# Optimization experiments

Measured on AMD Instinct MI355X. Metric: run time of the kernel, lower is better.

## Reference

```python
import jax, jax.numpy as jnp
import numpy as np

TAU = 2.0
SUR_ALPHA = 4.0  # spikingjelly surrogate.Sigmoid default alpha
LN_EPS = 1e-5
SCALE = 0.125
NUM_HEADS = 16


@jax.custom_vjp
def _spike(u):
    return (u >= 0.0).astype(u.dtype)

def _spike_fwd(u):
    return _spike(u), u

def _spike_bwd(u, g):
    s = jax.nn.sigmoid(SUR_ALPHA * u)
    return (g * SUR_ALPHA * s * (1.0 - s),)

_spike.defvjp(_spike_fwd, _spike_bwd)


def lif(x, v_th=1.0):
    # Single-step LIF from fresh state v=0, v_reset=0:
    # v_post = v + (x - v)/tau = x/tau; spike = H(v_post - v_th)
    return _spike(x / TAU - v_th)


def ln(x, g, b):
    m = jnp.mean(x, axis=-1, keepdims=True)
    v = jnp.var(x, axis=-1, keepdims=True)
    return (x - m) * jax.lax.rsqrt(v + LN_EPS) * g + b


def setup_inputs() -> dict:
    key = jax.random.key(0)
    ks = jax.random.split(key, 8)
    B, L, D = 4, 1024, 1024
    HID = 4096
    s_d = 1.0 / np.sqrt(D)
    s_h = 1.0 / np.sqrt(HID)
    return {
        "x": jax.random.normal(ks[0], (B, L, D), jnp.float32),
        "q_w": jax.random.normal(ks[1], (D, D), jnp.float32) * s_d,
        "q_g": jnp.ones((D,), jnp.float32),
        "q_b": jnp.zeros((D,), jnp.float32),
        "k_w": jax.random.normal(ks[2], (D, D), jnp.float32) * s_d,
        "k_g": jnp.ones((D,), jnp.float32),
        "k_b": jnp.zeros((D,), jnp.float32),
        "v_w": jax.random.normal(ks[3], (D, D), jnp.float32) * s_d,
        "v_g": jnp.ones((D,), jnp.float32),
        "v_b": jnp.zeros((D,), jnp.float32),
        "proj_w": jax.random.normal(ks[4], (D, D), jnp.float32) * s_d,
        "proj_bias": jnp.zeros((D,), jnp.float32),
        "proj_g": jnp.ones((D,), jnp.float32),
        "proj_beta": jnp.zeros((D,), jnp.float32),
        "fc1_w": jax.random.normal(ks[5], (D, HID), jnp.float32) * s_d,
        "fc1_bias": jnp.zeros((HID,), jnp.float32),
        "fc1_g": jnp.ones((HID,), jnp.float32),
        "fc1_beta": jnp.zeros((HID,), jnp.float32),
        "fc2_w": jax.random.normal(ks[6], (HID, D), jnp.float32) * s_h,
        "fc2_bias": jnp.zeros((D,), jnp.float32),
        "fc2_g": jnp.ones((D,), jnp.float32),
        "fc2_beta": jnp.zeros((D,), jnp.float32),
    }


def reference(x, q_w, q_g, q_b, k_w, k_g, k_b, v_w, v_g, v_b,
              proj_w, proj_bias, proj_g, proj_beta,
              fc1_w, fc1_bias, fc1_g, fc1_beta,
              fc2_w, fc2_bias, fc2_g, fc2_beta):
    B, L, D = x.shape
    H = NUM_HEADS
    hd = D // H

    # --- SSA ---
    q = lif(ln(x @ q_w, q_g, q_b))  # (B,L,D), binary spikes
    k = lif(ln(x @ k_w, k_g, k_b))
    v = lif(ln(x @ v_w, v_g, v_b))
    q = q.reshape(B, L, H, hd).transpose(0, 2, 1, 3)  # (B,H,L,hd)
    k = k.reshape(B, L, H, hd).transpose(0, 2, 1, 3)
    v = v.reshape(B, L, H, hd).transpose(0, 2, 1, 3)

    attn = jnp.einsum('bhqd,bhkd->bhqk', q, k) * SCALE  # no softmax
    y = jnp.einsum('bhqk,bhkd->bhqd', attn, v)
    y = y.transpose(0, 2, 1, 3).reshape(B, L, D)
    y = lif(y, v_th=0.5)                    # attn_lif (v_threshold=0.5)
    y = lif(ln(y @ proj_w + proj_bias, proj_g, proj_beta))

    x = x + y  # residual 1

    # --- MLP ---
    m = lif(ln(x @ fc1_w + fc1_bias, fc1_g, fc1_beta))
    m = lif(ln(m @ fc2_w + fc2_bias, fc2_g, fc2_beta))

    return x + m  # residual 2
```

## Files before the change

### kernel.cpp

```cpp
#include <hip/hip_runtime.h>
#include <hip/hip_bf16.h>


#define NB 4
#define LL 1024
#define DIM 1024
#define NH 16
#define HDIM 64
#define HID 4096
#define NROWS (NB * LL)

typedef unsigned short u16;
typedef __attribute__((ext_vector_type(8))) short short8v;
typedef __attribute__((ext_vector_type(4))) float f32x4;

__device__ __forceinline__ u16 f2bf(float f) {
    unsigned u = __builtin_bit_cast(unsigned, f);
    return (u16)((u + 0x7fffu + ((u >> 16) & 1u)) >> 16);
}
__device__ __forceinline__ float bf2f(u16 h) {
    unsigned u = ((unsigned)h) << 16;
    return __builtin_bit_cast(float, u);
}
__device__ __forceinline__ void split3v(float v, u16& a, u16& b, u16& c) {
    a = f2bf(v);
    float r = v - bf2f(a);
    b = f2bf(r);
    float r2 = r - bf2f(b);
    c = f2bf(r2);
}

__global__ __launch_bounds__(256) void split3_rows(
    const float* __restrict__ X, u16* __restrict__ Xs, int K)
{
    const int row = blockIdx.y;
    const int c4 = (blockIdx.x * 256 + threadIdx.x) * 4;
    if (c4 >= K) return;
    float4 v = *(const float4*)(X + (size_t)row * K + c4);
    float vv[4] = {v.x, v.y, v.z, v.w};
    u16 h0[4], h1[4], h2[4];
#pragma unroll
    for (int j = 0; j < 4; ++j) split3v(vv[j], h0[j], h1[j], h2[j]);
    u16* base = Xs + (size_t)row * 3 * K + c4;
    *(uint2*)(base + 0 * K) = *(uint2*)h0;
    *(uint2*)(base + 1 * K) = *(uint2*)h1;
    *(uint2*)(base + 2 * K) = *(uint2*)h2;
}

__global__ __launch_bounds__(256) void split_wt(
    const float* __restrict__ W, u16* __restrict__ Wt, int K, int N, int ldwt)
{
    __shared__ float tile[64][65];
    const int k0 = blockIdx.y * 64, n0 = blockIdx.x * 64;
    const int t = threadIdx.x;
    const int rr = t >> 4;
    const int cc = (t & 15) * 4;
#pragma unroll
    for (int it = 0; it < 4; ++it) {
        const int k = rr + it * 16;
        float4 v = *(const float4*)(W + (size_t)(k0 + k) * N + n0 + cc);
        tile[cc + 0][k] = v.x; tile[cc + 1][k] = v.y;
        tile[cc + 2][k] = v.z; tile[cc + 3][k] = v.w;
    }
    __syncthreads();
    const int n = t >> 2, kc = (t & 3) * 16;
    u16 h0[16], h1[16], h2[16];
#pragma unroll
    for (int j = 0; j < 16; ++j)
        split3v(tile[n][kc + j], h0[j], h1[j], h2[j]);
    u16* base = Wt + (size_t)(n0 + n) * ldwt + k0 + kc;
    *(uint4*)(base + 0 * K)     = ((uint4*)h0)[0];
    *(uint4*)(base + 0 * K + 8) = ((uint4*)h0)[1];
    *(uint4*)(base + 1 * K)     = ((uint4*)h1)[0];
    *(uint4*)(base + 1 * K + 8) = ((uint4*)h1)[1];
    *(uint4*)(base + 2 * K)     = ((uint4*)h2)[0];
    *(uint4*)(base + 2 * K + 8) = ((uint4*)h2)[1];
}

#define AS1G const __attribute__((address_space(1))) void*
#define AS3L __attribute__((address_space(3))) void*

__global__ __launch_bounds__(512, 2) void gemm256(
    const u16* __restrict__ A, int lda,
    const u16* __restrict__ Bt, int ldb,
    unsigned apack, unsigned bpack, int nt,
    const float* __restrict__ bias,
    float* __restrict__ Out, int ldo)
{
    __shared__ u16 As2[2][16384];
    __shared__ u16 Bs2[2][16384];
    const int t = threadIdx.x;
    const int wid = t >> 6, lane = t & 63;
    const int wm = wid >> 2, wn = wid & 3;
    const int row0 = blockIdx.y * 256, col0 = blockIdx.x * 256;
    const int lrow = lane & 15, lk = lane >> 4;
    const int sr0 = t >> 3;
    const int scol = ((t & 7) ^ (sr0 & 7)) * 8;

    f32x4 acc[8][4];
#pragma unroll
    for (int i = 0; i < 8; ++i)
#pragma unroll
        for (int j = 0; j < 4; ++j) acc[i][j] = f32x4{0.f, 0.f, 0.f, 0.f};

#define STA(bs, Rb, c0)                                                        \
    __builtin_amdgcn_global_load_lds(                                          \
        (AS1G)(A + (size_t)(row0 + (Rb) + sr0) * lda + (c0) + scol),           \
        (AS3L)(&As2[bs][(Rb) * 64 + t * 8]), 16, 0, 0);
#define STB(bs, Rb, c0)                                                        \
    {                                                                          \
        const int _rho = (Rb) + sr0;                                           \
        const int _bc = ((_rho >> 5) & 3) * 64 + ((_rho >> 7) << 5) + (_rho & 31); \
        __builtin_amdgcn_global_load_lds(                                      \
            (AS1G)(Bt + (size_t)(col0 + _bc) * ldb + (c0) + scol),             \
            (AS3L)(&Bs2[bs][(Rb) * 64 + t * 8]), 16, 0, 0);                    \
    }
#define STPAIR0(bs, cA, cB) STA(bs, 0, cA)   STA(bs, 128, cA)
#define STPAIR1(bs, cA, cB) STB(bs, 0, cB)   STB(bs, 64, cB)
#define STPAIR2(bs, cA, cB) STA(bs, 64, cA)  STA(bs, 192, cA)
#define STPAIR3(bs, cA, cB) STB(bs, 128, cB) STB(bs, 192, cB)

#define VMW(n) asm volatile("s_waitcnt vmcnt(" #n ")" ::: "memory");
#define BAR  __builtin_amdgcn_s_barrier();
#define BARP                                                                   \
    __builtin_amdgcn_s_barrier();                                              \
    __builtin_amdgcn_sched_barrier(0);

#define PHASE(MQ, NQ, P, STAGES)                                               \
    {                                                                          \
        short8v af[4][2], bf[2][2];                                            \
        _Pragma("unroll")                                                      \
        for (int mf = 0; mf < 4; ++mf) {                                       \
            const int r = wm * 128 + (MQ) * 64 + mf * 16 + lrow;               \
            _Pragma("unroll")                                                  \
            for (int ks = 0; ks < 2; ++ks) {                                   \
                const int slot = (lk + ks * 4) ^ (r & 7);                      \
                af[mf][ks] = *(const short8v*)&As2[P][r * 64 + slot * 8];      \
            }                                                                  \
        }                                                                      \
        _Pragma("unroll")                                                      \
        for (int nf = 0; nf < 2; ++nf) {                                       \
            const int rho = (NQ) * 128 + (wn >> 1) * 64 + (wn & 1) * 32        \
                            + nf * 16 + lrow;                                  \
            _Pragma("unroll")                                                  \
            for (int ks = 0; ks < 2; ++ks) {                                   \
                const int slot = (lk + ks * 4) ^ (rho & 7);                    \
                bf[nf][ks] = *(const short8v*)&Bs2[P][rho * 64 + slot * 8];    \
            }                                                                  \
        }                                                                      \
        STAGES                                                                 \
        asm volatile("s_waitcnt lgkmcnt(0)" ::: "memory");                     \
        __builtin_amdgcn_sched_barrier(0);                                     \
        __builtin_amdgcn_s_setprio(1);                                         \
        _Pragma("unroll")                                                      \
        for (int mf = 0; mf < 4; ++mf)                                         \
            _Pragma("unroll")                                                  \
            for (int nf = 0; nf < 2; ++nf)                                     \
                _Pragma("unroll")                                              \
                for (int ks = 0; ks < 2; ++ks)                                 \
                    acc[(MQ) * 4 + mf][(NQ) * 2 + nf] =                        \
                        __builtin_amdgcn_mfma_f32_16x16x32_bf16(               \
                            af[mf][ks], bf[nf][ks],                            \
                            acc[(MQ) * 4 + mf][(NQ) * 2 + nf], 0, 0, 0);       \
        __builtin_amdgcn_s_setprio(0);                                         \
    }
#define NOSTAGE ((void)0);

    {
        const int cA = (apack & 15) * 1024;
        const int cB = (bpack & 15) * 1024;
        STPAIR0(0, cA, cB) STPAIR1(0, cA, cB)
        STPAIR2(0, cA, cB) STPAIR3(0, cA, cB)
    }

    for (int kt = 0; kt < nt - 1; ++kt) {
        const int p = kt & 1, np = p ^ 1;
        const int nkt = kt + 1;
        const int nns = nkt >> 4, nk0 = (nkt & 15) * 64;
        const int nA = (int)((apack >> (nns * 4)) & 15) * 1024 + nk0;
        const int nB = (int)((bpack >> (nns * 4)) & 15) * 1024 + nk0;
        VMW(4) BARP PHASE(0, 0, p, STPAIR0(np, nA, nB))
        VMW(4) BAR  PHASE(1, 0, p, STPAIR1(np, nA, nB))
        VMW(4) BAR  PHASE(1, 1, p, STPAIR2(np, nA, nB))
        BAR         PHASE(0, 1, p, STPAIR3(np, nA, nB))
    }
    {
        const int p = (nt - 1) & 1;
        VMW(4) BARP PHASE(0, 0, p, NOSTAGE)
        VMW(2) BAR  PHASE(1, 0, p, NOSTAGE)
        VMW(0) BAR  PHASE(1, 1, p, NOSTAGE)
        BAR         PHASE(0, 1, p, NOSTAGE)
    }
#undef STA
#undef STB
#undef STPAIR0
#undef STPAIR1
#undef STPAIR2
#undef STPAIR3
#undef VMW
#undef BAR
#undef BARP
#undef PHASE
#undef NOSTAGE

#pragma unroll
    for (int ni = 0; ni < 4; ++ni) {
        const int col = col0 + wn * 64 + ni * 16 + lrow;
        const float bv = bias ? bias[col] : 0.f;
#pragma unroll
        for (int mi = 0; mi < 8; ++mi) {
            const int rbase = row0 + wm * 128 + mi * 16 + lk * 4;
#pragma unroll
            for (int r = 0; r < 4; ++r)
                Out[(size_t)(rbase + r) * ldo + col] = acc[mi][ni][r] + bv;
        }
    }
}

struct SegList { int a[6]; int b[6]; int n; };

template <int BN_>
__global__ __launch_bounds__(256) void gemm_mfma(
    const u16* __restrict__ A, int lda,
    const u16* __restrict__ Bt, int ldb,
    SegList segs, int Kseg,
    const float* __restrict__ bias,
    float* __restrict__ Out, int ldo)
{
    constexpr int NF = BN_ / 32;
    __shared__ u16 As[128 * 64];
    __shared__ u16 Bs[BN_ * 64];
    const int t = threadIdx.x;
    const int wid = t >> 6, lane = t & 63;
    const int wr = wid >> 1, wc = wid & 1;
    const int row0 = blockIdx.y * 128, col0 = blockIdx.x * BN_;
    const int lrow = lane & 15;
    const int s_subrow = lane >> 3;
    const int s_slot   = (lane & 7) ^ (lane >> 3);
    const int s_coff   = s_slot * 8;

    f32x4 acc[4][NF];
#pragma unroll
    for (int i = 0; i < 4; ++i)
#pragma unroll
        for (int j = 0; j < NF; ++j) acc[i][j] = f32x4{0.f, 0.f, 0.f, 0.f};

    for (int s = 0; s < segs.n; ++s) {
        const u16* pa = A + segs.a[s];
        const u16* pb = Bt + segs.b[s];
        for (int k0 = 0; k0 < Kseg; k0 += 64) {
            asm volatile("s_waitcnt lgkmcnt(0)" ::: "memory");
            __syncthreads();
#pragma unroll
            for (int c = 0; c < 4; ++c) {
                const int chunk = wid * 4 + c;
                const int rg = row0 + chunk * 8 + s_subrow;
                __builtin_amdgcn_global_load_lds(
                    (AS1G)(pa + (size_t)rg * lda + k0 + s_coff),
                    (AS3L)(&As[chunk * 512 + lane * 8]), 16, 0, 0);
            }
#pragma unroll
            for (int c = 0; c < NF; ++c) {
                const int chunk = wid * NF + c;
                const int rg = col0 + chunk * 8 + s_subrow;
                __builtin_amdgcn_global_load_lds(
                    (AS1G)(pb + (size_t)rg * ldb + k0 + s_coff),
                    (AS3L)(&Bs[chunk * 512 + lane * 8]), 16, 0, 0);
            }
            asm volatile("s_waitcnt vmcnt(0)" ::: "memory");
            __syncthreads();
#pragma unroll
            for (int ksub = 0; ksub < 2; ++ksub) {
                short8v af[4], bfr[NF];
#pragma unroll
                for (int f = 0; f < 4; ++f) {
                    const int ra = wr * 64 + f * 16 + lrow;
                    const int slot = ((lane >> 4) + ksub * 4) ^ (lrow & 7);
                    af[f] = *(const short8v*)&As[ra * 64 + slot * 8];
                }
#pragma unroll
                for (int f = 0; f < NF; ++f) {
                    const int rb = wc * (BN_ / 2) + f * 16 + lrow;
                    const int slot = ((lane >> 4) + ksub * 4) ^ (lrow & 7);
                    bfr[f] = *(const short8v*)&Bs[rb * 64 + slot * 8];
                }
#pragma unroll
                for (int i = 0; i < 4; ++i)
#pragma unroll
                    for (int j = 0; j < NF; ++j)
                        acc[i][j] = __builtin_amdgcn_mfma_f32_16x16x32_bf16(
                            af[i], bfr[j], acc[i][j], 0, 0, 0);
            }
        }
    }
#pragma unroll
    for (int j = 0; j < NF; ++j) {
        const int col = col0 + wc * (BN_ / 2) + j * 16 + lrow;
        const float bv = bias ? bias[col] : 0.f;
#pragma unroll
        for (int i = 0; i < 4; ++i) {
            const int rbase = row0 + wr * 64 + i * 16 + (lane >> 4) * 4;
#pragma unroll
            for (int r = 0; r < 4; ++r)
                Out[(size_t)(rbase + r) * ldo + col] = acc[i][j][r] + bv;
        }
    }
}

template <int DN>
__global__ __launch_bounds__(256) void lnlif2(
    const float* __restrict__ U, int ld, int coloff,
    const float* __restrict__ g, const float* __restrict__ beta,
    const float* __restrict__ resid,
    u16* __restrict__ spike_bf16,
    float* __restrict__ out_f32,
    u16* __restrict__ split3_out)
{
    constexpr int PT = DN / 1024;
    const int r = blockIdx.x, t = threadIdx.x;
    const float4* u4 = (const float4*)(U + (size_t)r * ld + coloff);
    float4 vals[PT];
    float lsum = 0.f;
#pragma unroll
    for (int i = 0; i < PT; ++i) {
        vals[i] = u4[t + i * 256];
        lsum += (vals[i].x + vals[i].y) + (vals[i].z + vals[i].w);
    }
    __shared__ float red[4];
    __shared__ float bcast;
    for (int o = 32; o > 0; o >>= 1) lsum += __shfl_down(lsum, o);
    if ((t & 63) == 0) red[t >> 6] = lsum;
    __syncthreads();
    if (t == 0) bcast = (red[0] + red[1] + red[2] + red[3]) * (1.f / DN);
    __syncthreads();
    const float m = bcast;
    float lss = 0.f;
#pragma unroll
    for (int i = 0; i < PT; ++i) {
        float dx = vals[i].x - m, dy = vals[i].y - m;
        float dz = vals[i].z - m, dw = vals[i].w - m;
        lss += (dx * dx + dy * dy) + (dz * dz + dw * dw);
    }
    for (int o = 32; o > 0; o >>= 1) lss += __shfl_down(lss, o);
    if ((t & 63) == 0) red[t >> 6] = lss;
    __syncthreads();
    if (t == 0) bcast = (red[0] + red[1] + red[2] + red[3]) * (1.f / DN);
    __syncthreads();
    const float rs = 1.f / sqrtf(bcast + 1e-5f);
#pragma unroll
    for (int i = 0; i < PT; ++i) {
        const int c = (t + i * 256) * 4;
        const size_t idx = (size_t)r * DN + c;
        const float4 gg = *(const float4*)(g + c);
        const float4 bb = *(const float4*)(beta + c);
        float sv[4];
        sv[0] = ((vals[i].x - m) * rs * gg.x + bb.x >= 2.0f) ? 1.f : 0.f;
        sv[1] = ((vals[i].y - m) * rs * gg.y + bb.y >= 2.0f) ? 1.f : 0.f;
        sv[2] = ((vals[i].z - m) * rs * gg.z + bb.z >= 2.0f) ? 1.f : 0.f;
        sv[3] = ((vals[i].w - m) * rs * gg.w + bb.w >= 2.0f) ? 1.f : 0.f;
        if (spike_bf16) {
            u16 sp[4];
#pragma unroll
            for (int j = 0; j < 4; ++j) sp[j] = sv[j] != 0.f ? (u16)0x3F80 : (u16)0;
            *(uint2*)(spike_bf16 + idx) = *(uint2*)sp;
        }
        if (out_f32 || split3_out) {
            float4 rv = resid ? *(const float4*)(resid + idx)
                              : float4{0.f, 0.f, 0.f, 0.f};
            float vv[4] = {rv.x + sv[0], rv.y + sv[1], rv.z + sv[2], rv.w + sv[3]};
            if (out_f32) {
                float4 ov = {vv[0], vv[1], vv[2], vv[3]};
                *(float4*)(out_f32 + idx) = ov;
            }
            if (split3_out) {
                u16 h0[4], h1[4], h2[4];
#pragma unroll
                for (int j = 0; j < 4; ++j) split3v(vv[j], h0[j], h1[j], h2[j]);
                u16* base = split3_out + (size_t)r * 3 * DN + c;
                *(uint2*)(base + 0 * DN) = *(uint2*)h0;
                *(uint2*)(base + 1 * DN) = *(uint2*)h1;
                *(uint2*)(base + 2 * DN) = *(uint2*)h2;
            }
        }
    }
}

__global__ __launch_bounds__(256) void ktv_part(
    const u16* __restrict__ Sk, const u16* __restrict__ Sv,
    float* __restrict__ ktvp)
{
    const int bh = blockIdx.x, ck = blockIdx.y;
    const int b = bh >> 4, h = bh & 15;
    __shared__ float kch[64][64];
    __shared__ float vch[64][64];
    const int t = threadIdx.x;
    const int i = t >> 2;
    const int j0 = (t & 3) << 4;
    float4 a0 = {0,0,0,0}, a1 = {0,0,0,0}, a2 = {0,0,0,0}, a3 = {0,0,0,0};
    for (int l0 = ck * 256; l0 < ck * 256 + 256; l0 += 64) {
        __syncthreads();
#pragma unroll
        for (int q = 0; q < 2; ++q) {
            const int chunk = t + q * 256;
            const int li = chunk >> 3, c8 = (chunk & 7) << 3;
            const size_t off = ((size_t)b * LL + l0 + li) * DIM + h * HDIM + c8;
            union { uint4 v; u16 s[8]; } uk, uv;
            uk.v = *(const uint4*)(Sk + off);
            uv.v = *(const uint4*)(Sv + off);
#pragma unroll
            for (int j = 0; j < 8; ++j) {
                kch[li][c8 + j] = uk.s[j] ? 1.f : 0.f;
                vch[li][c8 + j] = uv.s[j] ? 1.f : 0.f;
            }
        }
        __syncthreads();
        for (int l = 0; l < 64; ++l) {
            if (kch[l][i] != 0.f) {
                const float4 v0 = *(float4*)&vch[l][j0];
                const float4 v1 = *(float4*)&vch[l][j0 + 4];
                const float4 v2 = *(float4*)&vch[l][j0 + 8];
                const float4 v3 = *(float4*)&vch[l][j0 + 12];
                a0.x += v0.x; a0.y += v0.y; a0.z += v0.z; a0.w += v0.w;
                a1.x += v1.x; a1.y += v1.y; a1.z += v1.z; a1.w += v1.w;
                a2.x += v2.x; a2.y += v2.y; a2.z += v2.z; a2.w += v2.w;
                a3.x += v3.x; a3.y += v3.y; a3.z += v3.z; a3.w += v3.w;
            }
        }
    }
    const size_t o = (((size_t)ck * 64 + bh) * 64 + i) * 64 + j0;
    *(float4*)(ktvp + o)      = a0;
    *(float4*)(ktvp + o + 4)  = a1;
    *(float4*)(ktvp + o + 8)  = a2;
    *(float4*)(ktvp + o + 12) = a3;
}

__global__ __launch_bounds__(256) void qktv_bf16(
    const u16* __restrict__ Sq, const float* __restrict__ ktvp,
    u16* __restrict__ Y)
{
    const int bh = blockIdx.x, ck = blockIdx.y;
    const int b = bh >> 4, h = bh & 15;
    __shared__ float kt[64][64];
    const int t = threadIdx.x;
#pragma unroll
    for (int q = 0; q < 16; ++q) {
        const int idx = t + q * 256;
        ((float*)kt)[idx] = (ktvp[((size_t)0 * 64 + bh) * 4096 + idx]
                           + ktvp[((size_t)1 * 64 + bh) * 4096 + idx])
                          + (ktvp[((size_t)2 * 64 + bh) * 4096 + idx]
                           + ktvp[((size_t)3 * 64 + bh) * 4096 + idx]);
    }
    __syncthreads();
    const int li = t >> 6;
    const int j = t & 63;
    for (int l0 = ck * 128; l0 < ck * 128 + 128; l0 += 4) {
        const size_t roff = ((size_t)b * LL + l0 + li) * DIM + h * HDIM;
        const u16 sqv = Sq[roff + j];
        unsigned long long mask = __ballot(sqv != 0);
        float acc = 0.f;
        while (mask) {
            const int i = __ffsll((unsigned long long)mask) - 1;
            mask &= mask - 1;
            acc += kt[i][j];
        }
        const float y = 0.125f * acc;
        Y[roff + j] = (y >= 1.0f) ? (u16)0x3F80 : (u16)0;
    }
}

#define BM 128
#define BN 128
#define BK 16

__global__ __launch_bounds__(256) void gemm_f32(
    const float* __restrict__ A, const float* __restrict__ W,
    const float* __restrict__ bias, float* __restrict__ U,
    int M, int K, int N)
{
    __shared__ float As[BK][BM];
    __shared__ float Bs[BK][BN];
    const int t = threadIdx.x;
    const int tx = t & 15, ty = t >> 4;
    const int row0 = blockIdx.y * BM, col0 = blockIdx.x * BN;
    const int ar = t >> 2;
    const int ac = (t & 3) << 2;
    const int br = t >> 5;
    const int bc = (t & 31) << 2;
    float acc[8][8];
#pragma unroll
    for (int i = 0; i < 8; ++i)
#pragma unroll
        for (int j = 0; j < 8; ++j) acc[i][j] = 0.f;
    for (int k0 = 0; k0 < K; k0 += BK) {
        float4 va0 = *(const float4*)(A + (size_t)(row0 + ar) * K + k0 + ac);
        float4 va1 = *(const float4*)(A + (size_t)(row0 + ar + 64) * K + k0 + ac);
        float4 vb0 = *(const float4*)(W + (size_t)(k0 + br) * N + col0 + bc);
        float4 vb1 = *(const float4*)(W + (size_t)(k0 + br + 8) * N + col0 + bc);
        __syncthreads();
        As[ac + 0][ar] = va0.x; As[ac + 1][ar] = va0.y;
        As[ac + 2][ar] = va0.z; As[ac + 3][ar] = va0.w;
        As[ac + 0][ar + 64] = va1.x; As[ac + 1][ar + 64] = va1.y;
        As[ac + 2][ar + 64] = va1.z; As[ac + 3][ar + 64] = va1.w;
        *(float4*)&Bs[br][bc] = vb0;
        *(float4*)&Bs[br + 8][bc] = vb1;
        __syncthreads();
#pragma unroll
        for (int kk = 0; kk < BK; ++kk) {
            float4 fa0 = *(float4*)&As[kk][ty * 8];
            float4 fa1 = *(float4*)&As[kk][ty * 8 + 4];
            float4 fb0 = *(float4*)&Bs[kk][tx * 8];
            float4 fb1 = *(float4*)&Bs[kk][tx * 8 + 4];
            float av[8] = {fa0.x, fa0.y, fa0.z, fa0.w, fa1.x, fa1.y, fa1.z, fa1.w};
            float bv[8] = {fb0.x, fb0.y, fb0.z, fb0.w, fb1.x, fb1.y, fb1.z, fb1.w};
#pragma unroll
            for (int i = 0; i < 8; ++i)
#pragma unroll
                for (int j = 0; j < 8; ++j)
                    acc[i][j] += av[i] * bv[j];
        }
    }
    float bvals[8];
#pragma unroll
    for (int j = 0; j < 8; ++j)
        bvals[j] = bias ? bias[col0 + tx * 8 + j] : 0.f;
#pragma unroll
    for (int i = 0; i < 8; ++i) {
        const int row = row0 + ty * 8 + i;
        float* dst = U + (size_t)row * N + col0 + tx * 8;
        float4 o0, o1;
        o0.x = acc[i][0] + bvals[0]; o0.y = acc[i][1] + bvals[1];
        o0.z = acc[i][2] + bvals[2]; o0.w = acc[i][3] + bvals[3];
        o1.x = acc[i][4] + bvals[4]; o1.y = acc[i][5] + bvals[5];
        o1.z = acc[i][6] + bvals[6]; o1.w = acc[i][7] + bvals[7];
        *(float4*)dst = o0;
        *(float4*)(dst + 4) = o1;
    }
}

template <int DN>
__global__ __launch_bounds__(256) void lnlif_old(
    const float* __restrict__ U, const float* __restrict__ g,
    const float* __restrict__ beta, float thr,
    const float* __restrict__ resid, float* __restrict__ out)
{
    constexpr int PT = DN / 256;
    const int r = blockIdx.x, t = threadIdx.x;
    const float* u = U + (size_t)r * DN;
    float vals[PT];
    float lsum = 0.f;
#pragma unroll
    for (int i = 0; i < PT; ++i) { vals[i] = u[t + i * 256]; lsum += vals[i]; }
    __shared__ float red[4];
    __shared__ float bc0;
    for (int o = 32; o > 0; o >>= 1) lsum += __shfl_down(lsum, o);
    if ((t & 63) == 0) red[t >> 6] = lsum;
    __syncthreads();
    if (t == 0) bc0 = (red[0] + red[1] + red[2] + red[3]) * (1.f / DN);
    __syncthreads();
    const float m = bc0;
    float lss = 0.f;
#pragma unroll
    for (int i = 0; i < PT; ++i) { float d = vals[i] - m; lss += d * d; }
    for (int o = 32; o > 0; o >>= 1) lss += __shfl_down(lss, o);
    if ((t & 63) == 0) red[t >> 6] = lss;
    __syncthreads();
    if (t == 0) bc0 = (red[0] + red[1] + red[2] + red[3]) * (1.f / DN);
    __syncthreads();
    const float rs = 1.0f / sqrtf(bc0 + 1e-5f);
#pragma unroll
    for (int i = 0; i < PT; ++i) {
        const int c = t + i * 256;
        const float nrm = (vals[i] - m) * rs * g[c] + beta[c];
        const float s = (nrm >= thr) ? 1.0f : 0.0f;
        out[(size_t)r * DN + c] = resid ? (resid[(size_t)r * DN + c] + s) : s;
    }
}

__global__ __launch_bounds__(256) void ktv_f32(
    const float* __restrict__ Sk, const float* __restrict__ Sv,
    float* __restrict__ ktvb)
{
    const int bh = blockIdx.x;
    const int b = bh >> 4, h = bh & 15;
    __shared__ float kch[64][64];
    __shared__ float vch[64][64];
    const int t = threadIdx.x;
    const int i = t >> 2;
    const int j0 = (t & 3) << 4;
    float4 a0 = {0,0,0,0}, a1 = {0,0,0,0}, a2 = {0,0,0,0}, a3 = {0,0,0,0};
    for (int l0 = 0; l0 < LL; l0 += 64) {
        __syncthreads();
#pragma unroll
        for (int q = 0; q < 4; ++q) {
            const int idx = t + q * 256;
            const int li = idx >> 4, c4 = (idx & 15) << 2;
            const size_t off = ((size_t)b * LL + l0 + li) * DIM + h * HDIM + c4;
            *(float4*)&kch[li][c4] = *(const float4*)(Sk + off);
            *(float4*)&vch[li][c4] = *(const float4*)(Sv + off);
        }
        __syncthreads();
        for (int l = 0; l < 64; ++l) {
            if (kch[l][i] != 0.f) {
                const float4 v0 = *(float4*)&vch[l][j0];
                const float4 v1 = *(float4*)&vch[l][j0 + 4];
                const float4 v2 = *(float4*)&vch[l][j0 + 8];
                const float4 v3 = *(float4*)&vch[l][j0 + 12];
                a0.x += v0.x; a0.y += v0.y; a0.z += v0.z; a0.w += v0.w;
                a1.x += v1.x; a1.y += v1.y; a1.z += v1.z; a1.w += v1.w;
                a2.x += v2.x; a2.y += v2.y; a2.z += v2.z; a2.w += v2.w;
                a3.x += v3.x; a3.y += v3.y; a3.z += v3.z; a3.w += v3.w;
            }
        }
    }
    const size_t o = ((size_t)bh * 64 + i) * 64 + j0;
    *(float4*)(ktvb + o)      = a0;
    *(float4*)(ktvb + o + 4)  = a1;
    *(float4*)(ktvb + o + 8)  = a2;
    *(float4*)(ktvb + o + 12) = a3;
}

__global__ __launch_bounds__(256) void qktv_f32(
    const float* __restrict__ Sq, const float* __restrict__ ktvb,
    float* __restrict__ Y)
{
    const int bh = blockIdx.x;
    const int b = bh >> 4, h = bh & 15;
    __shared__ float kt[64][64];
    const int t = threadIdx.x;
#pragma unroll
    for (int q = 0; q < 16; ++q) {
        const int idx = t + q * 256;
        ((float*)kt)[idx] = ktvb[(size_t)bh * 4096 + idx];
    }
    __syncthreads();
    const int li = t >> 6;
    const int j = t & 63;
    for (int l0 = 0; l0 < LL; l0 += 4) {
        const size_t roff = ((size_t)b * LL + l0 + li) * DIM + h * HDIM;
        const float sqv = Sq[roff + j];
        unsigned long long mask = __ballot(sqv != 0.f);
        float acc = 0.f;
        while (mask) {
            const int i = __ffsll((unsigned long long)mask) - 1;
            mask &= mask - 1;
            acc += kt[i][j];
        }
        const float y = 0.125f * acc;
        Y[roff + j] = (y >= 1.0f) ? 1.0f : 0.0f;
    }
}

extern "C" void kernel_launch(void* const* d_in, const int* in_sizes, int n_in,
                              void* d_out, int out_size, void* d_ws, size_t ws_size,
                              hipStream_t stream)
{
    const float* x        = (const float*)d_in[0];
    const float* q_w      = (const float*)d_in[1];
    const float* q_g      = (const float*)d_in[2];
    const float* q_b      = (const float*)d_in[3];
    const float* k_w      = (const float*)d_in[4];
    const float* k_g      = (const float*)d_in[5];
    const float* k_b      = (const float*)d_in[6];
    const float* v_w      = (const float*)d_in[7];
    const float* v_g      = (const float*)d_in[8];
    const float* v_b      = (const float*)d_in[9];
    const float* proj_w   = (const float*)d_in[10];
    const float* proj_bias= (const float*)d_in[11];
    const float* proj_g   = (const float*)d_in[12];
    const float* proj_beta= (const float*)d_in[13];
    const float* fc1_w    = (const float*)d_in[14];
    const float* fc1_bias = (const float*)d_in[15];
    const float* fc1_g    = (const float*)d_in[16];
    const float* fc1_beta = (const float*)d_in[17];
    const float* fc2_w    = (const float*)d_in[18];
    const float* fc2_bias = (const float*)d_in[19];
    const float* fc2_g    = (const float*)d_in[20];
    const float* fc2_beta = (const float*)d_in[21];

    const dim3 blk(256);
    const size_t NEEDED = 143654912;

    if (ws_size >= NEEDED) {
        char* ws = (char*)d_ws;
        float* U    = (float*)ws;
        u16*   Xsh  = (u16*)(ws + 67108864);
        u16*   Wbuf = (u16*)(ws + 100663296);
        u16*   Sq   = (u16*)(ws + 125829120);
        u16*   Sk   = (u16*)(ws + 134217728);
        u16*   SvYb = (u16*)((char*)Xsh + 25165824);
        u16*   Xs   = Xsh;
        u16*   X1s  = Xsh;
        u16*   Sm   = Xsh;
        float* X1   = (float*)d_out;
        float* ktvp = (float*)(ws + 100663296);

        const int pa6[6] = {0, 1, 2, 0, 1, 0}, pb6[6] = {0, 1, 0, 2, 0, 1};
        unsigned apack = 0, bpack = 0;
        for (int i = 0; i < 6; ++i) {
            apack |= (unsigned)pa6[i] << (4 * i);
            bpack |= (unsigned)pb6[i] << (4 * i);
        }
        SegList segP;
        {
            for (int i = 0; i < 6; ++i) { segP.a[i] = 0; segP.b[i] = 0; }
            segP.b[1] = 1024; segP.b[2] = 2048; segP.n = 3;
        }
        SegList segF2;
        {
            for (int i = 0; i < 6; ++i) { segF2.a[i] = 0; segF2.b[i] = 0; }
            segF2.b[1] = 4096; segF2.b[2] = 8192; segF2.n = 3;
        }

        split3_rows<<<dim3(1, NROWS), blk, 0, stream>>>(x, Xs, DIM);

        split_wt<<<dim3(16, 16), blk, 0, stream>>>(q_w, Wbuf,               DIM, DIM, 3072);
        split_wt<<<dim3(16, 16), blk, 0, stream>>>(k_w, Wbuf + 1024 * 3072, DIM, DIM, 3072);
        split_wt<<<dim3(16, 16), blk, 0, stream>>>(v_w, Wbuf + 2048 * 3072, DIM, DIM, 3072);
        gemm256<<<dim3(12, 16), dim3(512), 0, stream>>>(
            Xs, 3072, Wbuf, 3072, apack, bpack, 96, nullptr, U, 3072);
        lnlif2<DIM><<<NROWS, blk, 0, stream>>>(U, 3072, 0,    q_g, q_b, nullptr, Sq,   nullptr, nullptr);
        lnlif2<DIM><<<NROWS, blk, 0, stream>>>(U, 3072, 1024, k_g, k_b, nullptr, Sk,   nullptr, nullptr);
        lnlif2<DIM><<<NROWS, blk, 0, stream>>>(U, 3072, 2048, v_g, v_b, nullptr, SvYb, nullptr, nullptr);

        ktv_part<<<dim3(NB * NH, 4), blk, 0, stream>>>(Sk, SvYb, ktvp);
        qktv_bf16<<<dim3(NB * NH, 8), blk, 0, stream>>>(Sq, ktvp, SvYb);

        split_wt<<<dim3(16, 16), blk, 0, stream>>>(proj_w, Wbuf, DIM, DIM, 3072);
        gemm_mfma<64><<<dim3(16, 32), blk, 0, stream>>>(SvYb, 1024, Wbuf, 3072, segP, 1024, proj_bias, U, DIM);
        lnlif2<DIM><<<NROWS, blk, 0, stream>>>(U, DIM, 0, proj_g, proj_beta, x, nullptr, X1, X1s);

        split_wt<<<dim3(64, 16), blk, 0, stream>>>(fc1_w, Wbuf, DIM, HID, 3072);
        gemm256<<<dim3(16, 16), dim3(512), 0, stream>>>(
            X1s, 3072, Wbuf, 3072, apack, bpack, 96, fc1_bias, U, HID);
        lnlif2<HID><<<NROWS, blk, 0, stream>>>(U, HID, 0, fc1_g, fc1_beta, nullptr, Sm, nullptr, nullptr);

        split_wt<<<dim3(16, 64), blk, 0, stream>>>(fc2_w, Wbuf, HID, DIM, 12288);
        gemm_mfma<64><<<dim3(16, 32), blk, 0, stream>>>(Sm, 4096, Wbuf, 12288, segF2, 4096, fc2_bias, U, DIM);
        lnlif2<DIM><<<NROWS, blk, 0, stream>>>(U, DIM, 0, fc2_g, fc2_beta, X1, nullptr, (float*)d_out, nullptr);
        return;
    }

    float* U    = (float*)d_ws;
    float* Sq   = U + (size_t)1 * NROWS * DIM;
    float* Sk   = U + (size_t)2 * NROWS * DIM;
    float* Sv   = U + (size_t)3 * NROWS * DIM;
    float* Yb   = Sv;
    float* ktvb = U + (size_t)NROWS * HID;
    float* Y2   = ktvb + (size_t)NB * NH * HDIM * HDIM;
    float* X1   = (float*)d_out;
    float* outf = (float*)d_out;

    const dim3 gemm_d(DIM / BN, NROWS / BM);
    const dim3 gemm_h(HID / BN, NROWS / BM);

    gemm_f32<<<gemm_d, blk, 0, stream>>>(x, q_w, nullptr, U, NROWS, DIM, DIM);
    lnlif_old<DIM><<<NROWS, blk, 0, stream>>>(U, q_g, q_b, 2.0f, nullptr, Sq);
    gemm_f32<<<gemm_d, blk, 0, stream>>>(x, k_w, nullptr, U, NROWS, DIM, DIM);
    lnlif_old<DIM><<<NROWS, blk, 0, stream>>>(U, k_g, k_b, 2.0f, nullptr, Sk);
    gemm_f32<<<gemm_d, blk, 0, stream>>>(x, v_w, nullptr, U, NROWS, DIM, DIM);
    lnlif_old<DIM><<<NROWS, blk, 0, stream>>>(U, v_g, v_b, 2.0f, nullptr, Sv);

    ktv_f32<<<NB * NH, blk, 0, stream>>>(Sk, Sv, ktvb);
    qktv_f32<<<NB * NH, blk, 0, stream>>>(Sq, ktvb, Yb);

    gemm_f32<<<gemm_d, blk, 0, stream>>>(Yb, proj_w, proj_bias, U, NROWS, DIM, DIM);
    lnlif_old<DIM><<<NROWS, blk, 0, stream>>>(U, proj_g, proj_beta, 2.0f, x, X1);

    gemm_f32<<<gemm_h, blk, 0, stream>>>(X1, fc1_w, fc1_bias, U, NROWS, DIM, HID);
    lnlif_old<HID><<<NROWS, blk, 0, stream>>>(U, fc1_g, fc1_beta, 2.0f, nullptr, U);

    gemm_f32<<<gemm_d, blk, 0, stream>>>(U, fc2_w, fc2_bias, Y2, NROWS, HID, DIM);
    lnlif_old<DIM><<<NROWS, blk, 0, stream>>>(Y2, fc2_g, fc2_beta, 2.0f, X1, outf);
}
```

Measured before the change: 691.0 us.

## Remap GEMM blocks across XCDs, reuse A fragments across phases, widen N tiles

Both GEMM kernels now remap the linear block id so that consecutive ids are spread across the 8 XCDs in contiguous chunks, to improve L2 locality on MI355X. The gemm256 phase loop keeps two A-fragment register sets and reorders phases so the A and B fragments already in registers are reused, cutting LDS reads per k-tile. The proj and fc2 GEMMs switch to a 128-wide N tile with half as many column blocks. The fragment reuse raises register pressure at 2 waves per SIMD, and the wider tile halves the grid, so occupancy and wave count may suffer.

```diff
diff --git a/kernel.cpp b/kernel.cpp
--- a/kernel.cpp
+++ b/kernel.cpp
@@ -92,7 +92,10 @@
     const int t = threadIdx.x;
     const int wid = t >> 6, lane = t & 63;
     const int wm = wid >> 2, wn = wid & 3;
-    const int row0 = blockIdx.y * 256, col0 = blockIdx.x * 256;
+    int bid = blockIdx.y * gridDim.x + blockIdx.x;
+    const int nwg = gridDim.x * gridDim.y;
+    bid = (bid & 7) * (nwg >> 3) + (bid >> 3);
+    const int row0 = (bid / gridDim.x) * 256, col0 = (bid % gridDim.x) * 256;
     const int lrow = lane & 15, lk = lane >> 4;
     const int sr0 = t >> 3;
     const int scol = ((t & 7) ^ (sr0 & 7)) * 8;
@@ -102,6 +105,7 @@
     for (int i = 0; i < 8; ++i)
 #pragma unroll
         for (int j = 0; j < 4; ++j) acc[i][j] = f32x4{0.f, 0.f, 0.f, 0.f};
+    short8v afA[4][2], afB[4][2], bf[2][2];
 
 #define STA(bs, Rb, c0)                                                        \
     __builtin_amdgcn_global_load_lds(                                          \
@@ -125,46 +129,44 @@
 #define BARP                                                                   \
     __builtin_amdgcn_s_barrier();                                              \
     __builtin_amdgcn_sched_barrier(0);
-
-#define PHASE(MQ, NQ, P, STAGES)                                               \
-    {                                                                          \
-        short8v af[4][2], bf[2][2];                                            \
+#define LGKM0                                                                  \
+    asm volatile("s_waitcnt lgkmcnt(0)" ::: "memory");                         \
+    __builtin_amdgcn_sched_barrier(0);
+
+#define LDA(dst, MQ, P)                                                        \
+    _Pragma("unroll")                                                          \
+    for (int mf = 0; mf < 4; ++mf) {                                           \
+        const int r = wm * 128 + (MQ) * 64 + mf * 16 + lrow;                   \
         _Pragma("unroll")                                                      \
-        for (int mf = 0; mf < 4; ++mf) {                                       \
-            const int r = wm * 128 + (MQ) * 64 + mf * 16 + lrow;               \
+        for (int ks = 0; ks < 2; ++ks) {                                       \
+            const int slot = (lk + ks * 4) ^ (r & 7);                          \
+            dst[mf][ks] = *(const short8v*)&As2[P][r * 64 + slot * 8];         \
+        }                                                                      \
+    }
+#define LDB(NQ, P)                                                             \
+    _Pragma("unroll")                                                          \
+    for (int nf = 0; nf < 2; ++nf) {                                           \
+        const int rho = (NQ) * 128 + (wn >> 1) * 64 + (wn & 1) * 32            \
+                        + nf * 16 + lrow;                                      \
+        _Pragma("unroll")                                                      \
+        for (int ks = 0; ks < 2; ++ks) {                                       \
+            const int slot = (lk + ks * 4) ^ (rho & 7);                        \
+            bf[nf][ks] = *(const short8v*)&Bs2[P][rho * 64 + slot * 8];        \
+        }                                                                      \
+    }
+#define MM(asrc, MQ, NQ)                                                       \
+    __builtin_amdgcn_s_setprio(1);                                             \
+    _Pragma("unroll")                                                          \
+    for (int mf = 0; mf < 4; ++mf)                                             \
+        _Pragma("unroll")                                                      \
+        for (int nf = 0; nf < 2; ++nf)                                         \
             _Pragma("unroll")                                                  \
-            for (int ks = 0; ks < 2; ++ks) {                                   \
-                const int slot = (lk + ks * 4) ^ (r & 7);                      \
-                af[mf][ks] = *(const short8v*)&As2[P][r * 64 + slot * 8];      \
-            }                                                                  \
-        }                                                                      \
-        _Pragma("unroll")                                                      \
-        for (int nf = 0; nf < 2; ++nf) {                                       \
-            const int rho = (NQ) * 128 + (wn >> 1) * 64 + (wn & 1) * 32        \
-                            + nf * 16 + lrow;                                  \
-            _Pragma("unroll")                                                  \
-            for (int ks = 0; ks < 2; ++ks) {                                   \
-                const int slot = (lk + ks * 4) ^ (rho & 7);                    \
-                bf[nf][ks] = *(const short8v*)&Bs2[P][rho * 64 + slot * 8];    \
-            }                                                                  \
-        }                                                                      \
-        STAGES                                                                 \
-        asm volatile("s_waitcnt lgkmcnt(0)" ::: "memory");                     \
-        __builtin_amdgcn_sched_barrier(0);                                     \
-        __builtin_amdgcn_s_setprio(1);                                         \
-        _Pragma("unroll")                                                      \
-        for (int mf = 0; mf < 4; ++mf)                                         \
-            _Pragma("unroll")                                                  \
-            for (int nf = 0; nf < 2; ++nf)                                     \
-                _Pragma("unroll")                                              \
-                for (int ks = 0; ks < 2; ++ks)                                 \
-                    acc[(MQ) * 4 + mf][(NQ) * 2 + nf] =                        \
-                        __builtin_amdgcn_mfma_f32_16x16x32_bf16(               \
-                            af[mf][ks], bf[nf][ks],                            \
-                            acc[(MQ) * 4 + mf][(NQ) * 2 + nf], 0, 0, 0);       \
-        __builtin_amdgcn_s_setprio(0);                                         \
-    }
-#define NOSTAGE ((void)0);
+            for (int ks = 0; ks < 2; ++ks)                                     \
+                acc[(MQ) * 4 + mf][(NQ) * 2 + nf] =                            \
+                    __builtin_amdgcn_mfma_f32_16x16x32_bf16(                   \
+                        asrc[mf][ks], bf[nf][ks],                              \
+                        acc[(MQ) * 4 + mf][(NQ) * 2 + nf], 0, 0, 0);           \
+    __builtin_amdgcn_s_setprio(0);
 
     {
         const int cA = (apack & 15) * 1024;
@@ -179,17 +181,21 @@
         const int nns = nkt >> 4, nk0 = (nkt & 15) * 64;
         const int nA = (int)((apack >> (nns * 4)) & 15) * 1024 + nk0;
         const int nB = (int)((bpack >> (nns * 4)) & 15) * 1024 + nk0;
-        VMW(4) BARP PHASE(0, 0, p, STPAIR0(np, nA, nB))
-        VMW(4) BAR  PHASE(1, 0, p, STPAIR1(np, nA, nB))
-        VMW(4) BAR  PHASE(1, 1, p, STPAIR2(np, nA, nB))
-        BAR         PHASE(0, 1, p, STPAIR3(np, nA, nB))
+        VMW(4) BARP
+        LDA(afA, 0, p) LDB(0, p) STPAIR0(np, nA, nB) LGKM0 MM(afA, 0, 0)
+        VMW(4) BAR
+        LDA(afB, 1, p) STPAIR1(np, nA, nB) LGKM0 MM(afB, 1, 0)
+        VMW(4) BAR
+        LDB(1, p) STPAIR2(np, nA, nB) LGKM0 MM(afB, 1, 1)
+        BAR
+        STPAIR3(np, nA, nB) MM(afA, 0, 1)
     }
     {
         const int p = (nt - 1) & 1;
-        VMW(4) BARP PHASE(0, 0, p, NOSTAGE)
-        VMW(2) BAR  PHASE(1, 0, p, NOSTAGE)
-        VMW(0) BAR  PHASE(1, 1, p, NOSTAGE)
-        BAR         PHASE(0, 1, p, NOSTAGE)
+        VMW(4) BARP LDA(afA, 0, p) LDB(0, p) LGKM0 MM(afA, 0, 0)
+        VMW(2) BAR  LDA(afB, 1, p) LGKM0 MM(afB, 1, 0)
+        VMW(0) BAR  LDB(1, p) LGKM0 MM(afB, 1, 1)
+        BAR         MM(afA, 0, 1)
     }
 #undef STA
 #undef STB
@@ -200,8 +206,10 @@
 #undef VMW
 #undef BAR
 #undef BARP
-#undef PHASE
-#undef NOSTAGE
+#undef LGKM0
+#undef LDA
+#undef LDB
+#undef MM
 
 #pragma unroll
     for (int ni = 0; ni < 4; ++ni) {
@@ -233,7 +241,10 @@
     const int t = threadIdx.x;
     const int wid = t >> 6, lane = t & 63;
     const int wr = wid >> 1, wc = wid & 1;
-    const int row0 = blockIdx.y * 128, col0 = blockIdx.x * BN_;
+    int bid = blockIdx.y * gridDim.x + blockIdx.x;
+    const int nwg = gridDim.x * gridDim.y;
+    bid = (bid & 7) * (nwg >> 3) + (bid >> 3);
+    const int row0 = (bid / gridDim.x) * 128, col0 = (bid % gridDim.x) * BN_;
     const int lrow = lane & 15;
     const int s_subrow = lane >> 3;
     const int s_slot   = (lane & 7) ^ (lane >> 3);
@@ -726,7 +737,7 @@
         qktv_bf16<<<dim3(NB * NH, 8), blk, 0, stream>>>(Sq, ktvp, SvYb);
 
         split_wt<<<dim3(16, 16), blk, 0, stream>>>(proj_w, Wbuf, DIM, DIM, 3072);
-        gemm_mfma<64><<<dim3(16, 32), blk, 0, stream>>>(SvYb, 1024, Wbuf, 3072, segP, 1024, proj_bias, U, DIM);
+        gemm_mfma<128><<<dim3(8, 32), blk, 0, stream>>>(SvYb, 1024, Wbuf, 3072, segP, 1024, proj_bias, U, DIM);
         lnlif2<DIM><<<NROWS, blk, 0, stream>>>(U, DIM, 0, proj_g, proj_beta, x, nullptr, X1, X1s);
 
         split_wt<<<dim3(64, 16), blk, 0, stream>>>(fc1_w, Wbuf, DIM, HID, 3072);
@@ -735,7 +746,7 @@
         lnlif2<HID><<<NROWS, blk, 0, stream>>>(U, HID, 0, fc1_g, fc1_beta, nullptr, Sm, nullptr, nullptr);
 
         split_wt<<<dim3(16, 64), blk, 0, stream>>>(fc2_w, Wbuf, HID, DIM, 12288);
-        gemm_mfma<64><<<dim3(16, 32), blk, 0, stream>>>(Sm, 4096, Wbuf, 12288, segF2, 4096, fc2_bias, U, DIM);
+        gemm_mfma<128><<<dim3(8, 32), blk, 0, stream>>>(Sm, 4096, Wbuf, 12288, segF2, 4096, fc2_bias, U, DIM);
         lnlif2<DIM><<<NROWS, blk, 0, stream>>>(U, DIM, 0, fc2_g, fc2_beta, X1, nullptr, (float*)d_out, nullptr);
         return;
     }
```

Measured after the change: 686.6 us. Within noise of the previous version (-0.6%).
